# Kernel optimization log

Measured on AMD Instinct MI355X. Metric: run time of the kernel, lower is better.

## Reference

```python
import jax, jax.numpy as jnp
import numpy as np

D = 768          # wav2vec2-base hidden size
H = 4            # cross-attn heads
HD = D // H
B = 8
N = 1024         # w2v sequence length (target length)
T = 2000         # raw CQCC frames
N_GAT = 3
NUM_CLASSES = 2


def _p(key, shape, scale=0.02):
    return jax.random.normal(key, shape, dtype=jnp.float32) * scale


def layer_norm(x, g, b, eps=1e-5):
    m = x.mean(-1, keepdims=True)
    v = x.var(-1, keepdims=True)
    return (x - m) * jax.lax.rsqrt(v + eps) * g + b


def gelu(x):
    return jax.nn.gelu(x, approximate=False)


def conv1d(x, w, b):
    # x [B,C,T], w [O,I,K], padding=1 (same)
    y = jax.lax.conv_general_dilated(x, w, (1,), [(1, 1)], dimension_numbers=('NCH', 'OIH', 'NCH'))
    return y + b[None, :, None]


def batchnorm(x, g, b, m, v, eps=1e-5):
    # eval-mode BatchNorm1d on [B,C,T]
    return (x - m[None, :, None]) * jax.lax.rsqrt(v[None, :, None] + eps) * g[None, :, None] + b[None, :, None]


def interp_linear(x, target_len):
    # torch F.interpolate(mode='linear', align_corners=False); x [B,T,D] -> [B,target_len,D]
    t_in = x.shape[1]
    pos = (jnp.arange(target_len, dtype=jnp.float32) + 0.5) * (t_in / target_len) - 0.5
    pos = jnp.clip(pos, 0.0, t_in - 1.0)
    lo = jnp.floor(pos).astype(jnp.int32)
    hi = jnp.minimum(lo + 1, t_in - 1)
    w = (pos - lo.astype(jnp.float32))[None, :, None]
    return x[:, lo] * (1.0 - w) + x[:, hi] * w


def mha(q, k, v, in_w, in_b, out_w, out_b):
    # torch nn.MultiheadAttention, batch_first=True
    bb, nq, _ = q.shape
    nk = k.shape[1]
    wq, wk, wv = in_w[:D], in_w[D:2 * D], in_w[2 * D:]
    bq, bk, bv = in_b[:D], in_b[D:2 * D], in_b[2 * D:]
    qh = (q @ wq.T + bq).reshape(bb, nq, H, HD).transpose(0, 2, 1, 3)
    kh = (k @ wk.T + bk).reshape(bb, nk, H, HD).transpose(0, 2, 1, 3)
    vh = (v @ wv.T + bv).reshape(bb, nk, H, HD).transpose(0, 2, 1, 3)
    scores = jnp.einsum('bhqd,bhkd->bhqk', qh, kh) * (1.0 / np.sqrt(HD))
    alpha = jax.nn.softmax(scores, axis=-1)
    o = jnp.einsum('bhqk,bhkd->bhqd', alpha, vh).transpose(0, 2, 1, 3).reshape(bb, nq, D)
    return o @ out_w.T + out_b


def graph_attn(x, fc_w, fc_b, a_w, a_b):
    # GAT score on concat([h_i, h_j]) decomposes additively: e_ij = a_i.h_i + a_j.h_j + b
    h = x @ fc_w.T + fc_b                      # [B,N,D]
    s_i = h @ a_w[:D]                          # [B,N]
    s_j = h @ a_w[D:]                          # [B,N]
    e = s_i[:, :, None] + s_j[:, None, :] + a_b  # [B,N,N]
    alpha = jax.nn.softmax(e, axis=-1)
    return jnp.einsum('bij,bjd->bid', alpha, h)


def _forward(w2v, cqcc, conv1_w, conv1_b, bn1_g, bn1_b, bn1_m, bn1_v,
             conv2_w, conv2_b, bn2_g, bn2_b, bn2_m, bn2_v, pos_embed,
             lnq_g, lnq_b, lnkv_g, lnkv_b,
             a1_in_w, a1_in_b, a1_out_w, a1_out_b,
             a2_in_w, a2_in_b, a2_out_w, a2_out_b,
             gat_fc_w, gat_fc_b, gat_a_w, gat_a_b, gln_g, gln_b,
             clf_w1, clf_b1, clf_w2, clf_b2):
    # CQCC conv stack
    x = gelu(batchnorm(conv1d(cqcc, conv1_w, conv1_b), bn1_g, bn1_b, bn1_m, bn1_v))
    x = gelu(batchnorm(conv1d(x, conv2_w, conv2_b), bn2_g, bn2_b, bn2_m, bn2_v))  # [B,D,T]
    cq = interp_linear(x.transpose(0, 2, 1), w2v.shape[1])  # [B,N,D]
    # shared positional encoding
    n = w2v.shape[1]
    w = w2v + pos_embed[:, :n]
    cq = cq + pos_embed[:, :n]
    # bidirectional cross attention (norm_q / norm_kv shared across directions)
    out1 = mha(layer_norm(cq, lnq_g, lnq_b), layer_norm(w, lnkv_g, lnkv_b),
               layer_norm(w, lnkv_g, lnkv_b), a1_in_w, a1_in_b, a1_out_w, a1_out_b)
    out2 = mha(layer_norm(w, lnq_g, lnq_b), layer_norm(cq, lnkv_g, lnkv_b),
               layer_norm(cq, lnkv_g, lnkv_b), a2_in_w, a2_in_b, a2_out_w, a2_out_b)
    x = out1 + out2
    # 3 residual graph-attention blocks
    for l in range(N_GAT):
        res = x
        x = graph_attn(x, gat_fc_w[l], gat_fc_b[l], gat_a_w[l], gat_a_b[l])
        x = layer_norm(x + res, gln_g[l], gln_b[l])
    pooled = x.mean(axis=1)
    h = gelu(pooled @ clf_w1.T + clf_b1)
    return h @ clf_w2.T + clf_b2


def setup_inputs():
    ks = iter(jax.random.split(jax.random.key(0), 64))
    inp = {}
    inp['w2v'] = jax.random.normal(next(ks), (B, N, D), dtype=jnp.float32)
    inp['cqcc'] = jax.random.normal(next(ks), (B, 20, T), dtype=jnp.float32)
    inp['conv1_w'] = _p(next(ks), (128, 20, 3)); inp['conv1_b'] = jnp.zeros((128,), jnp.float32)
    inp['bn1_g'] = jnp.ones((128,), jnp.float32); inp['bn1_b'] = jnp.zeros((128,), jnp.float32)
    inp['bn1_m'] = jnp.zeros((128,), jnp.float32); inp['bn1_v'] = jnp.ones((128,), jnp.float32)
    inp['conv2_w'] = _p(next(ks), (D, 128, 3)); inp['conv2_b'] = jnp.zeros((D,), jnp.float32)
    inp['bn2_g'] = jnp.ones((D,), jnp.float32); inp['bn2_b'] = jnp.zeros((D,), jnp.float32)
    inp['bn2_m'] = jnp.zeros((D,), jnp.float32); inp['bn2_v'] = jnp.ones((D,), jnp.float32)
    inp['pos_embed'] = _p(next(ks), (1, 2000, D), 1.0)
    inp['lnq_g'] = jnp.ones((D,), jnp.float32); inp['lnq_b'] = jnp.zeros((D,), jnp.float32)
    inp['lnkv_g'] = jnp.ones((D,), jnp.float32); inp['lnkv_b'] = jnp.zeros((D,), jnp.float32)
    inp['a1_in_w'] = _p(next(ks), (3 * D, D)); inp['a1_in_b'] = jnp.zeros((3 * D,), jnp.float32)
    inp['a1_out_w'] = _p(next(ks), (D, D)); inp['a1_out_b'] = jnp.zeros((D,), jnp.float32)
    inp['a2_in_w'] = _p(next(ks), (3 * D, D)); inp['a2_in_b'] = jnp.zeros((3 * D,), jnp.float32)
    inp['a2_out_w'] = _p(next(ks), (D, D)); inp['a2_out_b'] = jnp.zeros((D,), jnp.float32)
    inp['gat_fc_w'] = _p(next(ks), (N_GAT, D, D)); inp['gat_fc_b'] = jnp.zeros((N_GAT, D), jnp.float32)
    inp['gat_a_w'] = _p(next(ks), (N_GAT, 2 * D)); inp['gat_a_b'] = jnp.zeros((N_GAT,), jnp.float32)
    inp['gln_g'] = jnp.ones((N_GAT, D), jnp.float32); inp['gln_b'] = jnp.zeros((N_GAT, D), jnp.float32)
    inp['clf_w1'] = _p(next(ks), (128, D)); inp['clf_b1'] = jnp.zeros((128,), jnp.float32)
    inp['clf_w2'] = _p(next(ks), (NUM_CLASSES, 128)); inp['clf_b2'] = jnp.zeros((NUM_CLASSES,), jnp.float32)
    return inp


def reference(w2v, cqcc, conv1_w, conv1_b, bn1_g, bn1_b, bn1_m, bn1_v,
              conv2_w, conv2_b, bn2_g, bn2_b, bn2_m, bn2_v, pos_embed,
              lnq_g, lnq_b, lnkv_g, lnkv_b,
              a1_in_w, a1_in_b, a1_out_w, a1_out_b,
              a2_in_w, a2_in_b, a2_out_w, a2_out_b,
              gat_fc_w, gat_fc_b, gat_a_w, gat_a_b, gln_g, gln_b,
              clf_w1, clf_b1, clf_w2, clf_b2):
    return _forward(w2v, cqcc, conv1_w, conv1_b, bn1_g, bn1_b, bn1_m, bn1_v,
                    conv2_w, conv2_b, bn2_g, bn2_b, bn2_m, bn2_v, pos_embed,
                    lnq_g, lnq_b, lnkv_g, lnkv_b,
                    a1_in_w, a1_in_b, a1_out_w, a1_out_b,
                    a2_in_w, a2_in_b, a2_out_w, a2_out_b,
                    gat_fc_w, gat_fc_b, gat_a_w, gat_a_b, gln_g, gln_b,
                    clf_w1, clf_b1, clf_w2, clf_b2)
```

## Files before the change

kernel.cpp:

```cpp
#include <hip/hip_runtime.h>
#include <math.h>

#define DD 768
#define NH 4
#define HDIM 192
#define BBATCH 8
#define NSEQ 1024
#define TLEN 2000
#define SLOT 6291456
#define XROW 256256

typedef _Float16 h16;
typedef _Float16 half8v __attribute__((ext_vector_type(8)));
typedef _Float16 half4v __attribute__((ext_vector_type(4)));
typedef float f32x4 __attribute__((ext_vector_type(4)));

__device__ __forceinline__ float gelu_f(float x){
  return 0.5f * x * (1.0f + erff(x * 0.70710678118654752440f));
}
__device__ __forceinline__ float wave_sum(float v){
  #pragma unroll
  for (int off = 32; off; off >>= 1) v += __shfl_xor(v, off);
  return v;
}
__device__ __forceinline__ float wave_max(float v){
  #pragma unroll
  for (int off = 32; off; off >>= 1) v = fmaxf(v, __shfl_xor(v, off));
  return v;
}
__device__ __forceinline__ void gload16(const h16* g, h16* l){
  __builtin_amdgcn_global_load_lds(
      (const __attribute__((address_space(1))) void*)g,
      (__attribute__((address_space(3))) void*)l, 16, 0, 0);
}
__device__ __forceinline__ int xcd_remap(int orig, int nwg){
  int q = nwg >> 3, r = nwg & 7;
  int xcd = orig & 7, idx = orig >> 3;
  return (xcd < r ? xcd * (q + 1) : r * (q + 1) + (xcd - r) * q) + idx;
}

struct CastArgs {
  const float* s[5];
  h16* d[5];
  int cum[6];
};
__global__ __launch_bounds__(256) void k_cast5(CastArgs a, int total){
  int i = blockIdx.x * 256 + threadIdx.x;
  if (i >= total) return;
  int seg = 0;
  #pragma unroll
  for (int t = 1; t < 5; ++t) seg += (i >= a.cum[t]);
  int off = i - a.cum[seg];
  a.d[seg][off] = (h16)a.s[seg][off];
}

__global__ __launch_bounds__(256) void k_castc2(const float* __restrict__ s,
    h16* __restrict__ d){
  int i = blockIdx.x * 256 + threadIdx.x;
  if (i >= 294912) return;
  int oc = i / 384, rem = i % 384;
  int ic = rem / 3, kh = rem % 3;
  d[oc * 384 + kh * 128 + ic] = (h16)s[i];
}

__global__ __launch_bounds__(256) void k_conv1t(const float* __restrict__ cqcc,
    const float* __restrict__ w, const float* __restrict__ bias,
    const float* __restrict__ g, const float* __restrict__ be,
    const float* __restrict__ mm, const float* __restrict__ vv,
    h16* __restrict__ X){
  __shared__ float xs[20][258];
  __shared__ float wsm[32*60];
  const int t0 = blockIdx.x * 256;
  const int ocg = blockIdx.y, b = blockIdx.z;
  const int tid = threadIdx.x;
  for (int idx = tid; idx < 20*258; idx += 256){
    int ic = idx / 258, tt = idx % 258;
    int t = t0 + tt - 1;
    xs[ic][tt] = (t >= 0 && t < TLEN) ? cqcc[((size_t)b*20 + ic)*TLEN + t] : 0.f;
  }
  for (int idx = tid; idx < 32*60; idx += 256)
    wsm[idx] = w[ocg*32*60 + idx];
  __syncthreads();
  int t = t0 + tid;
  if (t >= TLEN) return;
  float acc[32] = {};
  for (int ic = 0; ic < 20; ++ic){
    float x0 = xs[ic][tid], x1v = xs[ic][tid+1], x2v = xs[ic][tid+2];
    #pragma unroll
    for (int oc = 0; oc < 32; ++oc){
      const float* wp = &wsm[(oc*20 + ic)*3];
      acc[oc] += wp[0]*x0 + wp[1]*x1v + wp[2]*x2v;
    }
  }
  h16* dst = X + (size_t)b*XROW + (size_t)(t+1)*128 + ocg*32;
  #pragma unroll 4
  for (int oc = 0; oc < 32; ++oc){
    int c = ocg*32 + oc;
    float s = rsqrtf(vv[c] + 1e-5f) * g[c];
    float val = (acc[oc] + bias[c] - mm[c]) * s + be[c];
    dst[oc] = (h16)gelu_f(val);
  }
  if (t == 0){
    h16* z = X + (size_t)b*XROW + ocg*32;
    #pragma unroll
    for (int oc = 0; oc < 32; ++oc) z[oc] = (h16)0.f;
  }
  if (t == TLEN-1){
    h16* z = X + (size_t)b*XROW + (size_t)2001*128 + ocg*32;
    #pragma unroll
    for (int oc = 0; oc < 32; ++oc) z[oc] = (h16)0.f;
  }
}

__global__ void k_bnprep(const float* __restrict__ cb, const float* __restrict__ g,
    const float* __restrict__ be, const float* __restrict__ m,
    const float* __restrict__ v, float* __restrict__ sc, float* __restrict__ off){
  int i = blockIdx.x * 256 + threadIdx.x;
  if (i >= DD) return;
  float s = g[i] * rsqrtf(v[i] + 1e-5f);
  sc[i] = s;
  off[i] = (cb[i] - m[i]) * s + be[i];
}

__global__ __launch_bounds__(256) void k_interp_ln(const h16* __restrict__ x2,
    const float* __restrict__ pe,
    const float* __restrict__ g1, const float* __restrict__ b1, h16* __restrict__ o1,
    const float* __restrict__ g2, const float* __restrict__ b2, h16* __restrict__ o2){
  __shared__ float ss[4], sqq[4];
  int row = blockIdx.x, tid = threadIdx.x;
  int b = row >> 10, i = row & 1023;
  float p = (i + 0.5f) * ((float)TLEN / (float)NSEQ) - 0.5f;
  p = fminf(fmaxf(p, 0.f), (float)(TLEN - 1));
  int lo = (int)floorf(p);
  int hi = min(lo + 1, TLEN - 1);
  float w = p - (float)lo;
  const h16* blo = x2 + ((size_t)b * TLEN + lo) * DD;
  const h16* bhi = x2 + ((size_t)b * TLEN + hi) * DD;
  const float* per = pe + (size_t)i * DD;
  float v[3]; float s = 0.f, sq = 0.f;
  #pragma unroll
  for (int j = 0; j < 3; ++j){
    int d = j * 256 + tid;
    float x = (float)blo[d] * (1.f - w) + (float)bhi[d] * w + per[d];
    v[j] = x; s += x; sq += x * x;
  }
  s = wave_sum(s); sq = wave_sum(sq);
  int wv = tid >> 6;
  if ((tid & 63) == 0){ ss[wv] = s; sqq[wv] = sq; }
  __syncthreads();
  s  = ss[0] + ss[1] + ss[2] + ss[3];
  sq = sqq[0] + sqq[1] + sqq[2] + sqq[3];
  float mean = s * (1.f / DD);
  float var  = sq * (1.f / DD) - mean * mean;
  float r = rsqrtf(var + 1e-5f);
  #pragma unroll
  for (int j = 0; j < 3; ++j){
    int d = j * 256 + tid;
    float xn = (v[j] - mean) * r;
    o1[(size_t)row * DD + d] = (h16)(xn * g1[d] + b1[d]);
    o2[(size_t)row * DD + d] = (h16)(xn * g2[d] + b2[d]);
  }
}

__global__ __launch_bounds__(256) void k_addpos_ln(const float* __restrict__ xin,
    const float* __restrict__ pe,
    const float* __restrict__ g1, const float* __restrict__ b1, h16* __restrict__ o1,
    const float* __restrict__ g2, const float* __restrict__ b2, h16* __restrict__ o2){
  __shared__ float ss[4], sqq[4];
  int row = blockIdx.x, tid = threadIdx.x;
  int i = row & 1023;
  const float* ip = xin + (size_t)row * DD;
  const float* per = pe + (size_t)i * DD;
  float v[3]; float s = 0.f, sq = 0.f;
  #pragma unroll
  for (int j = 0; j < 3; ++j){
    int d = j * 256 + tid;
    float x = ip[d] + per[d];
    v[j] = x; s += x; sq += x * x;
  }
  s = wave_sum(s); sq = wave_sum(sq);
  int wv = tid >> 6;
  if ((tid & 63) == 0){ ss[wv] = s; sqq[wv] = sq; }
  __syncthreads();
  s  = ss[0] + ss[1] + ss[2] + ss[3];
  sq = sqq[0] + sqq[1] + sqq[2] + sqq[3];
  float mean = s * (1.f / DD);
  float var  = sq * (1.f / DD) - mean * mean;
  float r = rsqrtf(var + 1e-5f);
  #pragma unroll
  for (int j = 0; j < 3; ++j){
    int d = j * 256 + tid;
    float xn = (v[j] - mean) * r;
    o1[(size_t)row * DD + d] = (h16)(xn * g1[d] + b1[d]);
    o2[(size_t)row * DD + d] = (h16)(xn * g2[d] + b2[d]);
  }
}

__global__ __launch_bounds__(256) void k_lnH(const h16* __restrict__ in,
    const float* __restrict__ ctx, const float* __restrict__ g,
    const float* __restrict__ be, h16* __restrict__ out){
  __shared__ float ss[4], sqq[4];
  int row = blockIdx.x, tid = threadIdx.x;
  const h16* ip = in + (size_t)row * DD;
  int b = row >> 10;
  float v[3]; float s = 0.f, sq = 0.f;
  #pragma unroll
  for (int j = 0; j < 3; ++j){
    int d = j * 256 + tid;
    float x = (float)ip[d] + ctx[b * DD + d];
    v[j] = x; s += x; sq += x * x;
  }
  s = wave_sum(s); sq = wave_sum(sq);
  int w = tid >> 6;
  if ((tid & 63) == 0){ ss[w] = s; sqq[w] = sq; }
  __syncthreads();
  s  = ss[0] + ss[1] + ss[2] + ss[3];
  sq = sqq[0] + sqq[1] + sqq[2] + sqq[3];
  float mean = s * (1.f / DD);
  float var  = sq * (1.f / DD) - mean * mean;
  float r = rsqrtf(var + 1e-5f);
  #pragma unroll
  for (int j = 0; j < 3; ++j){
    int d = j * 256 + tid;
    out[(size_t)row * DD + d] = (h16)((v[j] - mean) * r * g[d] + be[d]);
  }
}

__global__ __launch_bounds__(256) void k_addh(const h16* __restrict__ a,
    const h16* __restrict__ b, h16* __restrict__ o, int n8){
  int i = blockIdx.x * 256 + threadIdx.x;
  if (i < n8){
    half8v x = ((const half8v*)a)[i];
    half8v y = ((const half8v*)b)[i];
    ((half8v*)o)[i] = x + y;
  }
}

#define GEMM_MAINLOOP(Abase, lda, Wbase, ldw, Kdim)                          \
  auto stage = [&](int buf, int kt){                                         \
    _Pragma("unroll")                                                        \
    for (int i = 0; i < 4; ++i){                                             \
      int p = i*256 + tid; int row = p >> 3; int ch = (p & 7) ^ (row & 7);   \
      gload16(Abase + (size_t)(m0+row)*lda + kt + ch*8, &Als[buf][p*8]);     \
    }                                                                        \
    _Pragma("unroll")                                                        \
    for (int i = 0; i < 4; ++i){                                             \
      int p = i*256 + tid; int row = p >> 3; int ch = (p & 7) ^ (row & 7);   \
      gload16(Wbase + (size_t)(n0+row)*ldw + kt + ch*8, &Bls[buf][p*8]);     \
    }                                                                        \
  };                                                                         \
  stage(0, 0);                                                               \
  const int nk = Kdim >> 6;                                                  \
  for (int t = 0; t < nk; ++t){                                              \
    const int cur = t & 1;                                                   \
    if (t + 1 < nk){                                                         \
      stage(cur ^ 1, (t + 1) << 6);                                          \
      asm volatile("s_waitcnt vmcnt(8)" ::: "memory");                       \
    } else {                                                                 \
      asm volatile("s_waitcnt vmcnt(0)" ::: "memory");                       \
    }                                                                        \
    __builtin_amdgcn_s_barrier();                                            \
    __builtin_amdgcn_sched_barrier(0);                                       \
    __builtin_amdgcn_s_setprio(1);                                           \
    _Pragma("unroll")                                                        \
    for (int kk = 0; kk < 2; ++kk){                                          \
      half8v af[4], bf[4];                                                   \
      _Pragma("unroll")                                                      \
      for (int mi = 0; mi < 4; ++mi){                                        \
        int row = wr*64 + mi*16 + lr;                                        \
        int chp = (kk*4 + lg) ^ (row & 7);                                   \
        af[mi] = *(const half8v*)&Als[cur][row*64 + chp*8];                  \
      }                                                                      \
      _Pragma("unroll")                                                      \
      for (int ni = 0; ni < 4; ++ni){                                        \
        int row = wc*64 + ni*16 + lr;                                        \
        int chp = (kk*4 + lg) ^ (row & 7);                                   \
        bf[ni] = *(const half8v*)&Bls[cur][row*64 + chp*8];                  \
      }                                                                      \
      _Pragma("unroll")                                                      \
      for (int mi = 0; mi < 4; ++mi)                                         \
        _Pragma("unroll")                                                    \
        for (int ni = 0; ni < 4; ++ni)                                       \
          acc[mi][ni] = __builtin_amdgcn_mfma_f32_16x16x32_f16(              \
              af[mi], bf[ni], acc[mi][ni], 0, 0, 0);                         \
    }                                                                        \
    __builtin_amdgcn_s_setprio(0);                                           \
    asm volatile("s_waitcnt lgkmcnt(0)" ::: "memory");                       \
    __builtin_amdgcn_sched_barrier(0);                                       \
    __builtin_amdgcn_s_barrier();                                            \
  }

__global__ __launch_bounds__(256) void k_gemm_h(
    const h16* __restrict__ A, const h16* __restrict__ W,
    int lda, int ldw, int ldc, int K,
    const float* __restrict__ bias,
    h16* __restrict__ outh,
    const float* __restrict__ rdw, float* __restrict__ rdpart)
{
  __shared__ h16 Als[2][128*64];
  __shared__ h16 Bls[2][128*64];
  const int tid = threadIdx.x;
  const int gx = gridDim.x, gy = gridDim.y;
  const int wg = xcd_remap(blockIdx.x + gx * blockIdx.y, gx * gy);
  const int nidx = wg % gx;
  const int n0 = nidx * 128, m0 = (wg / gx) * 128;
  const int lane = tid & 63, wid = tid >> 6;
  const int wr = wid >> 1, wc = wid & 1;
  const int lr = lane & 15, lg = lane >> 4;
  f32x4 acc[4][4] = {};
  GEMM_MAINLOOP(A, lda, W, ldw, K)
  float rd[4][4] = {};
  #pragma unroll
  for (int mi = 0; mi < 4; ++mi){
    #pragma unroll
    for (int ni = 0; ni < 4; ++ni){
      int col = n0 + wc*64 + ni*16 + lr;
      int rowb = m0 + wr*64 + mi*16 + lg*4;
      float cb = bias[col];
      float aw = rdw ? rdw[col] : 0.f;
      #pragma unroll
      for (int r = 0; r < 4; ++r){
        size_t idx = (size_t)(rowb + r) * ldc + col;
        float v = acc[mi][ni][r] + cb;
        outh[idx] = (h16)v;
        if (rdw) rd[mi][r] += v * aw;
      }
    }
  }
  if (rdw){
    #pragma unroll
    for (int mi = 0; mi < 4; ++mi){
      #pragma unroll
      for (int r = 0; r < 4; ++r){
        float p = rd[mi][r];
        #pragma unroll
        for (int o = 1; o < 16; o <<= 1) p += __shfl_xor(p, o);
        if (lr == 0){
          int row = m0 + wr*64 + mi*16 + lg*4 + r;
          rdpart[(size_t)row * 12 + nidx*2 + wc] = p;
        }
      }
    }
  }
}

__global__ __launch_bounds__(256) void k_gemmop(
    const h16* __restrict__ A0, const h16* __restrict__ A1,
    const h16* __restrict__ W0, const h16* __restrict__ W1,
    const float* __restrict__ bb0, const float* __restrict__ bb1,
    h16* __restrict__ C0, h16* __restrict__ C1)
{
  __shared__ h16 Als[2][128*64];
  __shared__ h16 Bls[2][128*64];
  const int tid = threadIdx.x;
  const int gx = gridDim.x, gy = gridDim.y;
  const int nwg = gx * gy * 2;
  const int wg = xcd_remap(blockIdx.x + gx*(blockIdx.y + gy*blockIdx.z), nwg);
  const int n0 = (wg % gx) * 128;
  const int m0 = ((wg / gx) % gy) * 128;
  const int bz = wg / (gx * gy);
  const h16* A = bz ? A1 : A0;
  const h16* W = bz ? W1 : W0;
  const float* bias = bz ? bb1 : bb0;
  h16* C = bz ? C1 : C0;
  const int lane = tid & 63, wid = tid >> 6;
  const int wr = wid >> 1, wc = wid & 1;
  const int lr = lane & 15, lg = lane >> 4;
  f32x4 acc[4][4] = {};
  GEMM_MAINLOOP(A, DD, W, DD, DD)
  #pragma unroll
  for (int mi = 0; mi < 4; ++mi){
    #pragma unroll
    for (int ni = 0; ni < 4; ++ni){
      int col = n0 + wc*64 + ni*16 + lr;
      int rowb = m0 + wr*64 + mi*16 + lg*4;
      float cb = bias[col];
      #pragma unroll
      for (int r = 0; r < 4; ++r)
        C[(size_t)(rowb + r) * DD + col] = (h16)(acc[mi][ni][r] + cb);
    }
  }
}

__global__ __launch_bounds__(256) void k_conv2g(
    const h16* __restrict__ X, const h16* __restrict__ W,
    const float* __restrict__ sc, const float* __restrict__ off,
    h16* __restrict__ out)
{
  __shared__ h16 Als[2][128*64];
  __shared__ h16 Bls[2][128*64];
  const int tid = threadIdx.x;
  const int gx = gridDim.x, gy = gridDim.y;
  const int wg = xcd_remap(blockIdx.x + gx * blockIdx.y, gx * gy);
  const int n0 = (wg % gx) * 128, m0 = (wg / gx) * 128;
  const int lane = tid & 63, wid = tid >> 6;
  const int wr = wid >> 1, wc = wid & 1;
  const int lr = lane & 15, lg = lane >> 4;
  f32x4 acc[4][4] = {};
  auto stage = [&](int buf, int kt){
    #pragma unroll
    for (int i = 0; i < 4; ++i){
      int p = i*256 + tid; int row = p >> 3; int ch = (p & 7) ^ (row & 7);
      int rm = m0 + row, b = rm >> 11, t = rm & 2047;
      gload16(X + (size_t)b*XROW + (size_t)t*128 + kt + ch*8, &Als[buf][p*8]);
    }
    #pragma unroll
    for (int i = 0; i < 4; ++i){
      int p = i*256 + tid; int row = p >> 3; int ch = (p & 7) ^ (row & 7);
      gload16(W + (size_t)(n0+row)*384 + kt + ch*8, &Bls[buf][p*8]);
    }
  };
  stage(0, 0);
  const int nk = 6;
  for (int t = 0; t < nk; ++t){
    const int cur = t & 1;
    if (t + 1 < nk){
      stage(cur ^ 1, (t + 1) << 6);
      asm volatile("s_waitcnt vmcnt(8)" ::: "memory");
    } else {
      asm volatile("s_waitcnt vmcnt(0)" ::: "memory");
    }
    __builtin_amdgcn_s_barrier();
    __builtin_amdgcn_sched_barrier(0);
    __builtin_amdgcn_s_setprio(1);
    #pragma unroll
    for (int kk = 0; kk < 2; ++kk){
      half8v af[4], bf[4];
      #pragma unroll
      for (int mi = 0; mi < 4; ++mi){
        int row = wr*64 + mi*16 + lr;
        int chp = (kk*4 + lg) ^ (row & 7);
        af[mi] = *(const half8v*)&Als[cur][row*64 + chp*8];
      }
      #pragma unroll
      for (int ni = 0; ni < 4; ++ni){
        int row = wc*64 + ni*16 + lr;
        int chp = (kk*4 + lg) ^ (row & 7);
        bf[ni] = *(const half8v*)&Bls[cur][row*64 + chp*8];
      }
      #pragma unroll
      for (int mi = 0; mi < 4; ++mi)
        #pragma unroll
        for (int ni = 0; ni < 4; ++ni)
          acc[mi][ni] = __builtin_amdgcn_mfma_f32_16x16x32_f16(
              af[mi], bf[ni], acc[mi][ni], 0, 0, 0);
    }
    __builtin_amdgcn_s_setprio(0);
    asm volatile("s_waitcnt lgkmcnt(0)" ::: "memory");
    __builtin_amdgcn_sched_barrier(0);
    __builtin_amdgcn_s_barrier();
  }
  #pragma unroll
  for (int mi = 0; mi < 4; ++mi){
    #pragma unroll
    for (int ni = 0; ni < 4; ++ni){
      int col = n0 + wc*64 + ni*16 + lr;
      int rowb = m0 + wr*64 + mi*16 + lg*4;
      #pragma unroll
      for (int r = 0; r < 4; ++r){
        int rm = rowb + r, b = rm >> 11, t = rm & 2047;
        if (t < TLEN){
          float v = acc[mi][ni][r] * sc[col] + off[col];
          out[((size_t)b*TLEN + t)*DD + col] = (h16)gelu_f(v);
        }
      }
    }
  }
}

__global__ __launch_bounds__(256) void k_gemm6(
    const h16* __restrict__ Lall, const h16* __restrict__ w6,
    const float* __restrict__ b1, const float* __restrict__ b2,
    h16* __restrict__ qkv6)
{
  __shared__ h16 Als[2][128*64];
  __shared__ h16 Bls[2][128*64];
  const int tid = threadIdx.x;
  const int gx = gridDim.x, gy = gridDim.y;
  const int nwg = gx * gy * 6;
  const int wg = xcd_remap(blockIdx.x + gx*(blockIdx.y + gy*blockIdx.z), nwg);
  const int n0 = (wg % gx) * 128;
  const int m0 = ((wg / gx) % gy) * 128;
  const int bz = wg / (gx * gy);
  const int aidx = (1468 >> (2*bz)) & 3;
  const h16* A = Lall + (size_t)aidx * SLOT;
  const h16* W = w6 + (size_t)bz * 589824;
  const float* bias = (bz < 3 ? b1 + bz*DD : b2 + (bz-3)*DD);
  h16* C = qkv6 + (size_t)bz * SLOT;
  const int lane = tid & 63, wid = tid >> 6;
  const int wr = wid >> 1, wc = wid & 1;
  const int lr = lane & 15, lg = lane >> 4;
  f32x4 acc[4][4] = {};
  GEMM_MAINLOOP(A, DD, W, DD, DD)
  #pragma unroll
  for (int mi = 0; mi < 4; ++mi){
    #pragma unroll
    for (int ni = 0; ni < 4; ++ni){
      int col = n0 + wc*64 + ni*16 + lr;
      int rowb = m0 + wr*64 + mi*16 + lg*4;
      float cb = bias[col];
      #pragma unroll
      for (int r = 0; r < 4; ++r)
        C[(size_t)(rowb + r) * DD + col] = (h16)(acc[mi][ni][r] + cb);
    }
  }
}

__global__ __launch_bounds__(256) void k_trV(const h16* __restrict__ V0,
    const h16* __restrict__ V1, h16* __restrict__ VT0, h16* __restrict__ VT1){
  __shared__ h16 tile[64*64];
  const int zz = blockIdx.z;
  const int which = zz >> 5, bh = zz & 31;
  const int b = bh >> 2, h = bh & 3;
  const h16* Vh = which ? V1 : V0;
  h16* VT = which ? VT1 : VT0;
  const int q0 = blockIdx.x * 64, d0 = blockIdx.y * 64;
  const int t = threadIdx.x;
  {
    int qq = t >> 2, ds = (t & 3) * 16;
    const h16* src = Vh + ((size_t)b*NSEQ + q0 + qq)*DD + h*HDIM + d0 + ds;
    half8v v0 = *(const half8v*)src;
    half8v v1 = *(const half8v*)(src + 8);
    int c0 = (ds >> 3) ^ (qq & 7), c1 = ((ds >> 3) + 1) ^ (qq & 7);
    *(half8v*)&tile[qq*64 + c0*8] = v0;
    *(half8v*)&tile[qq*64 + c1*8] = v1;
  }
  __syncthreads();
  {
    int dd = t >> 2, qs = (t & 3) * 16;
    half8v o0, o1;
    #pragma unroll
    for (int j = 0; j < 8; ++j){
      int q = qs + j, q2 = qs + 8 + j;
      o0[j] = tile[q*64  + (((dd>>3) ^ (q&7))*8)  + (dd & 7)];
      o1[j] = tile[q2*64 + (((dd>>3) ^ (q2&7))*8) + (dd & 7)];
    }
    h16* dst = VT + (size_t)bh*HDIM*NSEQ + (size_t)(d0+dd)*NSEQ + q0 + qs;
    *(half8v*)dst = o0;
    *(half8v*)(dst + 8) = o1;
  }
}

__global__ __launch_bounds__(256) void k_flash(
    const h16* __restrict__ Q0, const h16* __restrict__ K0,
    const h16* __restrict__ T0, h16* __restrict__ O0,
    const h16* __restrict__ Q1, const h16* __restrict__ K1,
    const h16* __restrict__ T1, h16* __restrict__ O1){
  __shared__ h16 Ks[2][32*192];
  __shared__ h16 Vs[2][192*32];
  __shared__ h16 Ps[4][16*32];
  const int tid = threadIdx.x;
  const int bh = blockIdx.x, qt = blockIdx.y, which = blockIdx.z;
  const int b = bh >> 2, h = bh & 3;
  const int q0 = qt * 64;
  const h16* Qp = which ? Q1 : Q0;
  const h16* Kp = which ? K1 : K0;
  const h16* VTp = which ? T1 : T0;
  h16* Op = which ? O1 : O0;
  const h16* Qg = Qp + (size_t)b*NSEQ*DD + h*HDIM;
  const h16* Kg = Kp + (size_t)b*NSEQ*DD + h*HDIM;
  const h16* Vg = VTp + (size_t)bh*HDIM*NSEQ;
  const int lane = tid & 63, wid = tid >> 6;
  const int lr = lane & 15, lg = lane >> 4;
  half8v qf[6];
  {
    int qrow = q0 + wid*16 + lr;
    #pragma unroll
    for (int ks = 0; ks < 6; ++ks)
      qf[ks] = *(const half8v*)(Qg + (size_t)qrow*DD + ks*32 + lg*8);
  }
  auto stageK = [&](int buf, int k0){
    #pragma unroll
    for (int i = 0; i < 3; ++i){
      int p = i*256 + tid;
      int row = p / 24, chp = p % 24;
      int ch = chp ^ (row & 7);
      gload16(Kg + (size_t)(k0+row)*DD + ch*8, &Ks[buf][p*8]);
    }
  };
  auto stageV = [&](int buf, int k0){
    #pragma unroll
    for (int i = 0; i < 3; ++i){
      int p = i*256 + tid;
      int row = p >> 2, chp = p & 3;
      int ch = chp ^ ((row >> 1) & 3);
      gload16(Vg + (size_t)row*NSEQ + k0 + ch*8, &Vs[buf][p*8]);
    }
  };
  stageK(0, 0); stageV(0, 0);
  f32x4 oacc[12] = {};
  float m_run[4] = {-1e30f, -1e30f, -1e30f, -1e30f};
  float l_run[4] = {};
  const float SC = 0.07216878364870322f;
  __syncthreads();
  for (int kt = 0; kt < 32; ++kt){
    const int cur = kt & 1;
    if (kt + 1 < 32){ stageK(cur^1, (kt+1)*32); stageV(cur^1, (kt+1)*32); }
    f32x4 sacc[2] = {};
    __builtin_amdgcn_s_setprio(1);
    #pragma unroll
    for (int ks = 0; ks < 6; ++ks){
      #pragma unroll
      for (int t = 0; t < 2; ++t){
        int krow = t*16 + lr;
        int ch = (ks*4 + lg) ^ (krow & 7);
        half8v kf = *(const half8v*)&Ks[cur][krow*192 + ch*8];
        sacc[t] = __builtin_amdgcn_mfma_f32_16x16x32_f16(qf[ks], kf, sacc[t], 0, 0, 0);
      }
    }
    __builtin_amdgcn_s_setprio(0);
    float mnew[4], c[4], psum[4];
    #pragma unroll
    for (int r = 0; r < 4; ++r){
      float mt = fmaxf(sacc[0][r], sacc[1][r]);
      #pragma unroll
      for (int off = 1; off < 16; off <<= 1) mt = fmaxf(mt, __shfl_xor(mt, off));
      mnew[r] = fmaxf(m_run[r], mt * SC);
      c[r] = __expf(m_run[r] - mnew[r]);
      psum[r] = 0.f;
    }
    #pragma unroll
    for (int t = 0; t < 2; ++t){
      #pragma unroll
      for (int r = 0; r < 4; ++r){
        float p = __expf(sacc[t][r] * SC - mnew[r]);
        psum[r] += p;
        int q = lg*4 + r, key = t*16 + lr;
        int ch = (t*2 + (lr>>3)) ^ ((q>>1) & 3);
        Ps[wid][q*32 + ch*8 + (key & 7)] = (h16)p;
      }
    }
    #pragma unroll
    for (int r = 0; r < 4; ++r){
      #pragma unroll
      for (int off = 1; off < 16; off <<= 1) psum[r] += __shfl_xor(psum[r], off);
      l_run[r] = l_run[r] * c[r] + psum[r];
      m_run[r] = mnew[r];
    }
    #pragma unroll
    for (int dt = 0; dt < 12; ++dt){
      f32x4 o = oacc[dt];
      o[0] *= c[0]; o[1] *= c[1]; o[2] *= c[2]; o[3] *= c[3];
      oacc[dt] = o;
    }
    asm volatile("s_waitcnt lgkmcnt(0)" ::: "memory");
    __builtin_amdgcn_sched_barrier(0);
    {
      int pch = lg ^ ((lr >> 1) & 3);
      half8v pf = *(const half8v*)&Ps[wid][lr*32 + pch*8];
      __builtin_amdgcn_s_setprio(1);
      #pragma unroll
      for (int dt = 0; dt < 12; ++dt){
        int drow = dt*16 + lr;
        int vch = lg ^ ((drow >> 1) & 3);
        half8v vf = *(const half8v*)&Vs[cur][drow*32 + vch*8];
        oacc[dt] = __builtin_amdgcn_mfma_f32_16x16x32_f16(pf, vf, oacc[dt], 0, 0, 0);
      }
      __builtin_amdgcn_s_setprio(0);
    }
    __syncthreads();
  }
  float inv[4];
  #pragma unroll
  for (int r = 0; r < 4; ++r) inv[r] = 1.0f / l_run[r];
  h16* Og = Op + (size_t)b*NSEQ*DD + h*HDIM;
  #pragma unroll
  for (int dt = 0; dt < 12; ++dt){
    #pragma unroll
    for (int r = 0; r < 4; ++r){
      int q = q0 + wid*16 + lg*4 + r;
      Og[(size_t)q*DD + dt*16 + lr] = (h16)(oacc[dt][r] * inv[r]);
    }
  }
}

__global__ __launch_bounds__(256) void k_softmax12(const float* __restrict__ part,
    float* __restrict__ y){
  __shared__ float red[4];
  int b = blockIdx.x, tid = threadIdx.x;
  float v[4]; float mx = -1e30f;
  #pragma unroll
  for (int j = 0; j < 4; ++j){
    int i = j * 256 + tid;
    const float* p = part + (size_t)(b * NSEQ + i) * 12;
    float s = 0.f;
    #pragma unroll
    for (int k = 0; k < 12; ++k) s += p[k];
    v[j] = s; mx = fmaxf(mx, s);
  }
  mx = wave_max(mx);
  if ((tid & 63) == 0) red[tid >> 6] = mx;
  __syncthreads();
  mx = fmaxf(fmaxf(red[0], red[1]), fmaxf(red[2], red[3]));
  __syncthreads();
  float s = 0.f;
  #pragma unroll
  for (int j = 0; j < 4; ++j){ v[j] = __expf(v[j] - mx); s += v[j]; }
  s = wave_sum(s);
  if ((tid & 63) == 0) red[tid >> 6] = s;
  __syncthreads();
  s = red[0] + red[1] + red[2] + red[3];
  float inv = 1.0f / s;
  #pragma unroll
  for (int j = 0; j < 4; ++j) y[b * NSEQ + j * 256 + tid] = v[j] * inv;
}

__global__ __launch_bounds__(256) void k_ctx1(const float* __restrict__ alpha,
    const h16* __restrict__ h, float* __restrict__ part){
  int d = blockIdx.x * 256 + threadIdx.x;
  int b = blockIdx.y, pc = blockIdx.z;
  if (d >= DD) return;
  float acc = 0.f;
  const h16* hp = h + ((size_t)b * NSEQ + pc * 64) * DD + d;
  const float* ap = alpha + b * NSEQ + pc * 64;
  #pragma unroll 4
  for (int j = 0; j < 64; ++j) acc += ap[j] * (float)hp[(size_t)j * DD];
  part[(size_t)(b * 16 + pc) * DD + d] = acc;
}
__global__ __launch_bounds__(256) void k_ctx2(const float* __restrict__ part,
    float scale, float* __restrict__ ctx){
  int d = blockIdx.x * 256 + threadIdx.x;
  int b = blockIdx.y;
  if (d >= DD) return;
  float acc = 0.f;
  #pragma unroll
  for (int p = 0; p < 16; ++p) acc += part[(size_t)(b * 16 + p) * DD + d];
  ctx[b * DD + d] = acc * scale;
}

__global__ __launch_bounds__(256) void k_pool1(const h16* __restrict__ x,
    float* __restrict__ part){
  int d = blockIdx.x * 256 + threadIdx.x;
  int b = blockIdx.y, pc = blockIdx.z;
  if (d >= DD) return;
  float acc = 0.f;
  const h16* xp = x + ((size_t)b * NSEQ + pc * 64) * DD + d;
  #pragma unroll 4
  for (int j = 0; j < 64; ++j) acc += (float)xp[(size_t)j * DD];
  part[(size_t)(b * 16 + pc) * DD + d] = acc;
}

__global__ __launch_bounds__(128) void k_clf(const float* __restrict__ pooled,
    const float* __restrict__ w1, const float* __restrict__ b1,
    const float* __restrict__ w2, const float* __restrict__ b2,
    float* __restrict__ out){
  __shared__ float pl[DD];
  __shared__ float h1[128];
  int b = blockIdx.x, tid = threadIdx.x;
  #pragma unroll
  for (int j = 0; j < 6; ++j) pl[j * 128 + tid] = pooled[b * DD + j * 128 + tid];
  __syncthreads();
  float acc = b1[tid];
  const float* wp = w1 + (size_t)tid * DD;
  for (int d = 0; d < DD; ++d) acc += pl[d] * wp[d];
  h1[tid] = gelu_f(acc);
  __syncthreads();
  if (tid < 2){
    float o = b2[tid];
    const float* w2p = w2 + tid * 128;
    for (int c = 0; c < 128; ++c) o += h1[c] * w2p[c];
    out[b * 2 + tid] = o;
  }
}

extern "C" void kernel_launch(void* const* d_in, const int* in_sizes, int n_in,
                              void* d_out, int out_size, void* d_ws, size_t ws_size,
                              hipStream_t stream){
  (void)in_sizes; (void)n_in; (void)out_size;
  const float* w2v      = (const float*)d_in[0];
  const float* cqcc     = (const float*)d_in[1];
  const float* conv1_w  = (const float*)d_in[2];
  const float* conv1_b  = (const float*)d_in[3];
  const float* bn1_g    = (const float*)d_in[4];
  const float* bn1_b    = (const float*)d_in[5];
  const float* bn1_m    = (const float*)d_in[6];
  const float* bn1_v    = (const float*)d_in[7];
  const float* conv2_w  = (const float*)d_in[8];
  const float* conv2_b  = (const float*)d_in[9];
  const float* bn2_g    = (const float*)d_in[10];
  const float* bn2_b    = (const float*)d_in[11];
  const float* bn2_m    = (const float*)d_in[12];
  const float* bn2_v    = (const float*)d_in[13];
  const float* pos_embed= (const float*)d_in[14];
  const float* lnq_g    = (const float*)d_in[15];
  const float* lnq_b    = (const float*)d_in[16];
  const float* lnkv_g   = (const float*)d_in[17];
  const float* lnkv_b   = (const float*)d_in[18];
  const float* a1_in_w  = (const float*)d_in[19];
  const float* a1_in_b  = (const float*)d_in[20];
  const float* a1_out_w = (const float*)d_in[21];
  const float* a1_out_b = (const float*)d_in[22];
  const float* a2_in_w  = (const float*)d_in[23];
  const float* a2_in_b  = (const float*)d_in[24];
  const float* a2_out_w = (const float*)d_in[25];
  const float* a2_out_b = (const float*)d_in[26];
  const float* gat_fc_w = (const float*)d_in[27];
  const float* gat_fc_b = (const float*)d_in[28];
  const float* gat_a_w  = (const float*)d_in[29];
  const float* gln_g    = (const float*)d_in[31];
  const float* gln_b    = (const float*)d_in[32];
  const float* clf_w1   = (const float*)d_in[33];
  const float* clf_b1   = (const float*)d_in[34];
  const float* clf_w2   = (const float*)d_in[35];
  const float* clf_b2   = (const float*)d_in[36];

  char* wsp = (char*)d_ws;
  auto F = [&](size_t bytes){ char* p = wsp; wsp += (bytes + 255) & ~(size_t)255; return p; };
  h16* xh      = (h16*)F(12582912);
  h16* Lall    = (h16*)F(4*12582912);
  h16* qkv6    = (h16*)F(6*12582912);
  h16* VT      = (h16*)F(12582912);
  h16* VT2     = (h16*)F(12582912);
  h16* o1h     = (h16*)F(12582912);
  h16* o2h     = (h16*)F(12582912);
  h16* w6      = (h16*)F(2*3538944);
  h16* w_a1out = (h16*)F(1179648);
  h16* w_a2out = (h16*)F(1179648);
  h16* w_gat   = (h16*)F(3538944);
  h16* w_c2    = (h16*)F(589824);
  float* scb   = (float*)F(3072);
  float* offb  = (float*)F(3072);
  float* alpha = (float*)F(32768);
  float* ctxb  = (float*)F(24576);
  float* pooled= (float*)F(24576);
  float* partb = (float*)F(393216);
  if ((size_t)(wsp - (char*)d_ws) > ws_size) return;

  h16* X   = Lall;
  h16* x2h = qkv6;
  h16* hh  = qkv6;

  const int NR = BBATCH * NSEQ;

  {
    CastArgs ca;
    ca.s[0]=a1_in_w;  ca.d[0]=w6;            int n0=1769472;
    ca.s[1]=a2_in_w;  ca.d[1]=w6+1769472;    int n1=1769472;
    ca.s[2]=a1_out_w; ca.d[2]=w_a1out;       int n2=589824;
    ca.s[3]=a2_out_w; ca.d[3]=w_a2out;       int n3=589824;
    ca.s[4]=gat_fc_w; ca.d[4]=w_gat;         int n4=1769472;
    ca.cum[0]=0; ca.cum[1]=n0; ca.cum[2]=n0+n1; ca.cum[3]=n0+n1+n2;
    ca.cum[4]=n0+n1+n2+n3; ca.cum[5]=n0+n1+n2+n3+n4;
    int total = ca.cum[5];
    k_cast5<<<(total+255)/256, 256, 0, stream>>>(ca, total);
  }
  k_castc2<<<(294912+255)/256, 256, 0, stream>>>(conv2_w, w_c2);
  k_bnprep<<<3, 256, 0, stream>>>(conv2_b, bn2_g, bn2_b, bn2_m, bn2_v, scb, offb);

  k_conv1t<<<dim3(8, 4, BBATCH), 256, 0, stream>>>(cqcc, conv1_w, conv1_b,
      bn1_g, bn1_b, bn1_m, bn1_v, X);
  k_conv2g<<<dim3(6, 128), 256, 0, stream>>>(X, w_c2, scb, offb, x2h);

  k_interp_ln<<<NR, 256, 0, stream>>>(x2h, pos_embed,
      lnq_g, lnq_b, Lall, lnkv_g, lnkv_b, Lall + SLOT);
  k_addpos_ln<<<NR, 256, 0, stream>>>(w2v, pos_embed,
      lnq_g, lnq_b, Lall + 2*SLOT, lnkv_g, lnkv_b, Lall + 3*SLOT);

  k_gemm6<<<dim3(6, 64, 6), 256, 0, stream>>>(Lall, w6, a1_in_b, a2_in_b, qkv6);

  k_trV<<<dim3(16, 3, 64), 256, 0, stream>>>(qkv6 + 2*(size_t)SLOT,
      qkv6 + 5*(size_t)SLOT, VT, VT2);
  k_flash<<<dim3(32, 16, 2), 256, 0, stream>>>(
      qkv6, qkv6 + (size_t)SLOT, VT, qkv6,
      qkv6 + 3*(size_t)SLOT, qkv6 + 4*(size_t)SLOT, VT2,
      qkv6 + 3*(size_t)SLOT);
  k_gemmop<<<dim3(6, 64, 2), 256, 0, stream>>>(
      qkv6, qkv6 + 3*(size_t)SLOT, w_a1out, w_a2out,
      a1_out_b, a2_out_b, o1h, o2h);
  k_addh<<<(NR*DD/8 + 255)/256, 256, 0, stream>>>(o1h, o2h, xh, NR*DD/8);

  for (int l = 0; l < 3; ++l){
    k_gemm_h<<<dim3(6, 64), 256, 0, stream>>>(xh, w_gat + (size_t)l*589824,
        DD, DD, DD, DD, gat_fc_b + l*DD, hh, gat_a_w + l*2*DD + DD, partb);
    k_softmax12<<<BBATCH, 256, 0, stream>>>(partb, alpha);
    k_ctx1<<<dim3(3, BBATCH, 16), 256, 0, stream>>>(alpha, hh, partb);
    k_ctx2<<<dim3(3, BBATCH), 256, 0, stream>>>(partb, 1.0f, ctxb);
    k_lnH<<<NR, 256, 0, stream>>>(xh, ctxb, gln_g + l*DD, gln_b + l*DD, xh);
  }

  k_pool1<<<dim3(3, BBATCH, 16), 256, 0, stream>>>(xh, partb);
  k_ctx2<<<dim3(3, BBATCH), 256, 0, stream>>>(partb, 1.0f/NSEQ, pooled);
  k_clf<<<BBATCH, 128, 0, stream>>>(pooled, clf_w1, clf_b1, clf_w2, clf_b2,
                                    (float*)d_out);
}
```

Baseline: 582.6 us.

## Overlap K/V prefetch via vmcnt waits and lazily rescale softmax in exp2 domain

In the flash-attention loop, `__syncthreads` is replaced by explicit waits and barriers. The loop now waits with `vmcnt(6)` only for the current tile's loads, so the next tile's global-to-LDS loads stay in flight during compute. The online softmax moves to the base-2 domain by folding log2(e) into the scale. The running max and the 12 output accumulators are rescaled only when the new tile max exceeds the running max by a threshold, which skips most per-tile rescale multiplies. The cost is larger unnormalized probabilities stored in fp16 (bounded by the threshold) and more fragile hand-written synchronization.

```diff
diff --git a/kernel.cpp b/kernel.cpp
--- a/kernel.cpp
+++ b/kernel.cpp
@@ -589,13 +589,20 @@
   };
   stageK(0, 0); stageV(0, 0);
   f32x4 oacc[12] = {};
-  float m_run[4] = {-1e30f, -1e30f, -1e30f, -1e30f};
+  float m2[4] = {-1e30f, -1e30f, -1e30f, -1e30f};
   float l_run[4] = {};
-  const float SC = 0.07216878364870322f;
-  __syncthreads();
+  const float SC2 = 0.07216878364870322f * 1.4426950408889634f;
+  const float TH2 = 11.5415603f;
   for (int kt = 0; kt < 32; ++kt){
     const int cur = kt & 1;
-    if (kt + 1 < 32){ stageK(cur^1, (kt+1)*32); stageV(cur^1, (kt+1)*32); }
+    if (kt + 1 < 32){
+      stageK(cur^1, (kt+1)*32); stageV(cur^1, (kt+1)*32);
+      asm volatile("s_waitcnt vmcnt(6)" ::: "memory");
+    } else {
+      asm volatile("s_waitcnt vmcnt(0)" ::: "memory");
+    }
+    __builtin_amdgcn_s_barrier();
+    __builtin_amdgcn_sched_barrier(0);
     f32x4 sacc[2] = {};
     __builtin_amdgcn_s_setprio(1);
     #pragma unroll
@@ -609,21 +616,25 @@
       }
     }
     __builtin_amdgcn_s_setprio(0);
-    float mnew[4], c[4], psum[4];
+    float c[4]; bool any = false;
     #pragma unroll
     for (int r = 0; r < 4; ++r){
       float mt = fmaxf(sacc[0][r], sacc[1][r]);
       #pragma unroll
       for (int off = 1; off < 16; off <<= 1) mt = fmaxf(mt, __shfl_xor(mt, off));
-      mnew[r] = fmaxf(m_run[r], mt * SC);
-      c[r] = __expf(m_run[r] - mnew[r]);
-      psum[r] = 0.f;
-    }
+      float pm2 = mt * SC2;
+      if (pm2 > m2[r] + TH2){
+        c[r] = exp2f(m2[r] - pm2);
+        m2[r] = pm2;
+        any = true;
+      } else c[r] = 1.f;
+    }
+    float psum[4] = {};
     #pragma unroll
     for (int t = 0; t < 2; ++t){
       #pragma unroll
       for (int r = 0; r < 4; ++r){
-        float p = __expf(sacc[t][r] * SC - mnew[r]);
+        float p = exp2f(sacc[t][r] * SC2 - m2[r]);
         psum[r] += p;
         int q = lg*4 + r, key = t*16 + lr;
         int ch = (t*2 + (lr>>3)) ^ ((q>>1) & 3);
@@ -635,13 +646,14 @@
       #pragma unroll
       for (int off = 1; off < 16; off <<= 1) psum[r] += __shfl_xor(psum[r], off);
       l_run[r] = l_run[r] * c[r] + psum[r];
-      m_run[r] = mnew[r];
-    }
-    #pragma unroll
-    for (int dt = 0; dt < 12; ++dt){
-      f32x4 o = oacc[dt];
-      o[0] *= c[0]; o[1] *= c[1]; o[2] *= c[2]; o[3] *= c[3];
-      oacc[dt] = o;
+    }
+    if (any){
+      #pragma unroll
+      for (int dt = 0; dt < 12; ++dt){
+        f32x4 o = oacc[dt];
+        o[0] *= c[0]; o[1] *= c[1]; o[2] *= c[2]; o[3] *= c[3];
+        oacc[dt] = o;
+      }
     }
     asm volatile("s_waitcnt lgkmcnt(0)" ::: "memory");
     __builtin_amdgcn_sched_barrier(0);
@@ -658,7 +670,9 @@
       }
       __builtin_amdgcn_s_setprio(0);
     }
-    __syncthreads();
+    asm volatile("s_waitcnt lgkmcnt(0)" ::: "memory");
+    __builtin_amdgcn_sched_barrier(0);
+    __builtin_amdgcn_s_barrier();
   }
   float inv[4];
   #pragma unroll
```

Result: no change. 573.4 us (-1.6%).
